# Performance work log

Measured on AMD Instinct MI355X. Metric: run time of the kernel, lower is better.

Reference implementation:

```python
import jax, jax.numpy as jnp
import numpy as np

NEG_SLOPE = 0.2

def _gat_layer(x, src, dst, W, a_s, a_d, b, concat):
    # x: [N, F_in], W: [F_in, H*C], a_s/a_d: [H, C]
    N = x.shape[0]
    H, C = a_s.shape
    h = (x @ W).reshape(N, H, C)                       # per-head projection
    al_s = jnp.sum(h * a_s, axis=-1)                   # [N, H]
    al_d = jnp.sum(h * a_d, axis=-1)                   # [N, H]
    e = jax.nn.leaky_relu(al_s[src] + al_d[dst], NEG_SLOPE)  # [E, H]
    # segment softmax over incoming edges of each dst node
    m = jax.ops.segment_max(e, dst, num_segments=N)    # [N, H]
    ex = jnp.exp(e - m[dst])
    denom = jax.ops.segment_sum(ex, dst, num_segments=N)
    alpha = ex / denom[dst]                            # [E, H]
    msg = h[src] * alpha[:, :, None]                   # [E, H, C]
    out = jax.ops.segment_sum(msg, dst, num_segments=N)  # [N, H, C]
    if concat:
        return out.reshape(N, H * C) + b
    return out.mean(axis=1) + b


def setup_inputs() -> dict:
    key = jax.random.key(0)
    ks = jax.random.split(key, 12)
    N, F_in, H, C1, LAT, E = 16384, 512, 4, 128, 64, 262144
    x = jax.random.normal(ks[0], (N, F_in), dtype=jnp.float32)
    edge_index = jax.random.randint(ks[1], (2, E), 0, N, dtype=jnp.int64)
    s = 0.05
    return {
        'x': x,
        'edge_index': edge_index,
        'W1': jax.random.normal(ks[2], (F_in, H * C1), dtype=jnp.float32) * s,
        'a_src1': jax.random.normal(ks[3], (H, C1), dtype=jnp.float32) * s,
        'a_dst1': jax.random.normal(ks[4], (H, C1), dtype=jnp.float32) * s,
        'b1': jax.random.normal(ks[5], (H * C1,), dtype=jnp.float32) * s,
        'W2': jax.random.normal(ks[6], (H * C1, H * LAT), dtype=jnp.float32) * s,
        'a_src2': jax.random.normal(ks[7], (H, LAT), dtype=jnp.float32) * s,
        'a_dst2': jax.random.normal(ks[8], (H, LAT), dtype=jnp.float32) * s,
        'b2': jax.random.normal(ks[9], (LAT,), dtype=jnp.float32) * s,
    }


def reference(x, edge_index, W1, a_src1, a_dst1, b1, W2, a_src2, a_dst2, b2):
    N = x.shape[0]
    # PyG GATConv default add_self_loops=True
    loop = jnp.arange(N, dtype=edge_index.dtype)
    src = jnp.concatenate([edge_index[0], loop])
    dst = jnp.concatenate([edge_index[1], loop])
    h = jax.nn.relu(_gat_layer(x, src, dst, W1, a_src1, a_dst1, b1, concat=True))
    out = _gat_layer(h, src, dst, W2, a_src2, a_dst2, b2, concat=False)
    return out
```

## Files before the change

### kernel.cpp

```cpp
#include <hip/hip_runtime.h>
#include <stdint.h>
#include <stddef.h>
#include <limits.h>

typedef __bf16 bf16;
typedef __bf16 bf16x4 __attribute__((ext_vector_type(4)));
typedef __bf16 bf16x8 __attribute__((ext_vector_type(8)));
typedef float  f32x4  __attribute__((ext_vector_type(4)));

#define CAP 128

static __device__ __forceinline__ float lrelu(float x) { return x > 0.f ? x : 0.2f * x; }
static __device__ __forceinline__ float san(float v) { return (fabsf(v) < 1e4f) ? v : 0.0f; }
static __device__ __forceinline__ float wexp(float e) { return __expf(fminf(e, 30.f)); }

static __device__ __forceinline__ void async_load16(const bf16* g, bf16* l) {
  __builtin_amdgcn_global_load_lds((const __attribute__((address_space(1))) void*)g,
                                   (__attribute__((address_space(3))) void*)l, 16, 0, 0);
}

static __device__ __forceinline__ void drain_barrier() {
  asm volatile("s_waitcnt vmcnt(0) lgkmcnt(0)" ::: "memory");
  __builtin_amdgcn_s_barrier();
}


__global__ __launch_bounds__(256) void prep_w(int* __restrict__ cnt,
                                              const float* __restrict__ W1,
                                              const float* __restrict__ W2,
                                              bf16* __restrict__ W1T,
                                              bf16* __restrict__ W2T,
                                              int N) {
  int b = blockIdx.x;
  if (b < N / 256) { cnt[b * 256 + threadIdx.x] = 0; return; }
  b -= N / 256;
  __shared__ bf16 t[32][33];
  const float* in; bf16* out; int R, C, bx, by;
  if (b < 256) { in = W1; out = W1T; R = 512; C = 512; by = b >> 4; bx = b & 15; }
  else         { b -= 256; in = W2; out = W2T; R = 512; C = 256; by = b >> 3; bx = b & 7; }
  const int lane = threadIdx.x & 31, r8 = threadIdx.x >> 5;
#pragma unroll
  for (int k = 0; k < 4; ++k) {
    int r = by * 32 + r8 + k * 8, c = bx * 32 + lane;
    t[lane][r8 + k * 8] = (bf16)san(in[(size_t)r * C + c]);
  }
  __syncthreads();
#pragma unroll
  for (int k = 0; k < 4; ++k) {
    int oc = bx * 32 + r8 + k * 8;
    out[(size_t)oc * R + by * 32 + lane] = t[r8 + k * 8][lane];
  }
}


__global__ __launch_bounds__(256) void gemm_al_l1(const float* __restrict__ X,
                                                  const bf16* __restrict__ BT,
                                                  bf16* __restrict__ C,
                                                  const float* __restrict__ a_s,
                                                  const float* __restrict__ a_d,
                                                  float* __restrict__ al_s,
                                                  float* __restrict__ al_d,
                                                  const int* __restrict__ src,
                                                  const int* __restrict__ dst,
                                                  int E, int* __restrict__ cnt,
                                                  int* __restrict__ slots,
                                                  int M, int N, int K) {
  __shared__ __align__(16) bf16 As[2][64 * 32];
  __shared__ __align__(16) bf16 Bs[2][128 * 32];
  __shared__ float alred[2][64][2];
  const int tid = threadIdx.x;
  const int b   = blockIdx.x;

  if (b >= 1024) {
    for (int e = (b - 1024) * 256 + tid; e < E; e += 256 * 256) {
      int d = dst[e];
      int pos = atomicAdd(&cnt[d], 1);
      if (pos < CAP) slots[(size_t)d * CAP + pos] = src[e];
    }
    return;
  }

  const int lane = tid & 63;
  const int wave = tid >> 6;
  const int m0 = (b & 255) * 64;
  const int head = b >> 8;
  const int n0 = head * 128;
  const int wm = (wave >> 1) * 32;
  const int wn = (wave & 1) * 64;

  f32x4 acc[2][4] = {};

  const int id1 = tid + 256;
  const float* apx = X  + (size_t)(m0 + (tid >> 2)) * K + (tid & 3) * 8;
  const bf16*  b0p = BT + (size_t)(n0 + (tid >> 2)) * K + (tid & 3) * 8;
  const bf16*  b1p = BT + (size_t)(n0 + (id1 >> 2)) * K + (id1 & 3) * 8;

  const int kq = (lane >> 4) * 8;
  const int rA = wm + (lane & 15);
  const int rB = wn + (lane & 15);

  {
    async_load16(b0p, &Bs[0][tid * 8]);
    async_load16(b1p, &Bs[0][id1 * 8]);
    f32x4 u0 = *(const f32x4*)(apx);
    f32x4 u1 = *(const f32x4*)(apx + 4);
    bf16x8 w;
#pragma unroll
    for (int k = 0; k < 4; ++k) { w[k] = (bf16)san(u0[k]); w[4 + k] = (bf16)san(u1[k]); }
    *(bf16x8*)&As[0][tid * 8] = w;
    drain_barrier();
  }

  int cur = 0;
  for (int k0 = 0; k0 < K; k0 += 32) {
    const int kn = k0 + 32;
    const bool pf = (kn < K);
    f32x4 u0, u1;
    if (pf) {
      async_load16(b0p + kn, &Bs[cur ^ 1][tid * 8]);
      async_load16(b1p + kn, &Bs[cur ^ 1][id1 * 8]);
      u0 = *(const f32x4*)(apx + kn);
      u1 = *(const f32x4*)(apx + kn + 4);
    }

    bf16x8 af[2], bfv[4];
#pragma unroll
    for (int i = 0; i < 2; ++i) af[i]  = *(const bf16x8*)&As[cur][(rA + i * 16) * 32 + kq];
#pragma unroll
    for (int j = 0; j < 4; ++j) bfv[j] = *(const bf16x8*)&Bs[cur][(rB + j * 16) * 32 + kq];
#pragma unroll
    for (int i = 0; i < 2; ++i)
#pragma unroll
      for (int j = 0; j < 4; ++j)
        acc[i][j] = __builtin_amdgcn_mfma_f32_16x16x32_bf16(af[i], bfv[j], acc[i][j], 0, 0, 0);

    if (pf) {
      bf16x8 w;
#pragma unroll
      for (int k = 0; k < 4; ++k) { w[k] = (bf16)san(u0[k]); w[4 + k] = (bf16)san(u1[k]); }
      *(bf16x8*)&As[cur ^ 1][tid * 8] = w;
    }

    drain_barrier();
    cur ^= 1;
  }

  const int cc = lane & 15;
  const int rb = (lane >> 4) * 4;
#pragma unroll
  for (int i = 0; i < 2; ++i)
#pragma unroll
    for (int j = 0; j < 4; ++j) {
      int gcol = n0 + wn + j * 16 + cc;
#pragma unroll
      for (int r = 0; r < 4; ++r) {
        int grow = m0 + wm + i * 16 + rb + r;
        C[(size_t)grow * N + gcol] = (bf16)acc[i][j][r];
      }
    }

  {
    float asv[4], adv[4];
#pragma unroll
    for (int j = 0; j < 4; ++j) {
      int col = head * 128 + wn + j * 16 + cc;
      asv[j] = san(a_s[col]);
      adv[j] = san(a_d[col]);
    }
    const int wnh = wn >> 6;
#pragma unroll
    for (int i = 0; i < 2; ++i)
#pragma unroll
      for (int r = 0; r < 4; ++r) {
        float ps = 0.f, pd = 0.f;
#pragma unroll
        for (int j = 0; j < 4; ++j) { ps += acc[i][j][r] * asv[j]; pd += acc[i][j][r] * adv[j]; }
#pragma unroll
        for (int off = 1; off <= 8; off <<= 1) {
          ps += __shfl_xor(ps, off);
          pd += __shfl_xor(pd, off);
        }
        if (cc == 0) {
          int row = wm + i * 16 + rb + r;
          alred[wnh][row][0] = ps;
          alred[wnh][row][1] = pd;
        }
      }
    __syncthreads();
    if (tid < 64) {
      al_s[(size_t)(m0 + tid) * 4 + head] = alred[0][tid][0] + alred[1][tid][0];
      al_d[(size_t)(m0 + tid) * 4 + head] = alred[0][tid][1] + alred[1][tid][1];
    }
  }
}


__global__ __launch_bounds__(256) void gemm_al_l2(const bf16* __restrict__ A,
                                                  const bf16* __restrict__ BT,
                                                  bf16* __restrict__ C,
                                                  const float* __restrict__ a_s,
                                                  const float* __restrict__ a_d,
                                                  float* __restrict__ al_s,
                                                  float* __restrict__ al_d,
                                                  int M, int N, int K) {
  __shared__ __align__(16) bf16 As[2][64 * 32];
  __shared__ __align__(16) bf16 Bs[2][128 * 32];
  const int tid  = threadIdx.x;
  const int lane = tid & 63;
  const int wave = tid >> 6;
  const int m0 = blockIdx.x * 64;
  const int n0 = blockIdx.y * 128;
  const int wm = (wave >> 1) * 32;
  const int wn = (wave & 1) * 64;

  f32x4 acc[2][4] = {};

  const int tb = tid + 256;
  const bf16* ap  = A  + (size_t)(m0 + (tid >> 2)) * K + (tid & 3) * 8;
  const bf16* bp0 = BT + (size_t)(n0 + (tid >> 2)) * K + (tid & 3) * 8;
  const bf16* bp1 = BT + (size_t)(n0 + (tb  >> 2)) * K + (tb  & 3) * 8;

  const int kq = (lane >> 4) * 8;
  const int rA = wm + (lane & 15);
  const int rB = wn + (lane & 15);

  async_load16(ap,  &As[0][tid * 8]);
  async_load16(bp0, &Bs[0][tid * 8]);
  async_load16(bp1, &Bs[0][tb  * 8]);
  drain_barrier();

  int cur = 0;
  for (int k0 = 0; k0 < K; k0 += 32) {
    const int kn = k0 + 32;
    if (kn < K) {
      async_load16(ap  + kn, &As[cur ^ 1][tid * 8]);
      async_load16(bp0 + kn, &Bs[cur ^ 1][tid * 8]);
      async_load16(bp1 + kn, &Bs[cur ^ 1][tb  * 8]);
    }

    bf16x8 af[2], bfv[4];
#pragma unroll
    for (int i = 0; i < 2; ++i) af[i]  = *(const bf16x8*)&As[cur][(rA + i * 16) * 32 + kq];
#pragma unroll
    for (int j = 0; j < 4; ++j) bfv[j] = *(const bf16x8*)&Bs[cur][(rB + j * 16) * 32 + kq];
#pragma unroll
    for (int i = 0; i < 2; ++i)
#pragma unroll
      for (int j = 0; j < 4; ++j)
        acc[i][j] = __builtin_amdgcn_mfma_f32_16x16x32_bf16(af[i], bfv[j], acc[i][j], 0, 0, 0);

    drain_barrier();
    cur ^= 1;
  }

  const int cc = lane & 15;
  const int rb = (lane >> 4) * 4;
#pragma unroll
  for (int i = 0; i < 2; ++i)
#pragma unroll
    for (int j = 0; j < 4; ++j) {
      int gcol = n0 + wn + j * 16 + cc;
#pragma unroll
      for (int r = 0; r < 4; ++r) {
        int grow = m0 + wm + i * 16 + rb + r;
        C[(size_t)grow * N + gcol] = (bf16)acc[i][j][r];
      }
    }

  {
    const int head = blockIdx.y * 2 + (wn >> 6);
    float asv[4], adv[4];
#pragma unroll
    for (int j = 0; j < 4; ++j) {
      int col = head * 64 + j * 16 + cc;
      asv[j] = san(a_s[col]);
      adv[j] = san(a_d[col]);
    }
#pragma unroll
    for (int i = 0; i < 2; ++i)
#pragma unroll
      for (int r = 0; r < 4; ++r) {
        float ps = 0.f, pd = 0.f;
#pragma unroll
        for (int j = 0; j < 4; ++j) { ps += acc[i][j][r] * asv[j]; pd += acc[i][j][r] * adv[j]; }
#pragma unroll
        for (int off = 1; off <= 8; off <<= 1) {
          ps += __shfl_xor(ps, off);
          pd += __shfl_xor(pd, off);
        }
        if (cc == 0) {
          int row = m0 + wm + i * 16 + rb + r;
          al_s[(size_t)row * 4 + head] = ps;
          al_d[(size_t)row * 4 + head] = pd;
        }
      }
  }
}


__global__ __launch_bounds__(256) void aggregate1_f(const bf16* __restrict__ h1,
                                                    const float* __restrict__ al_s,
                                                    const float* __restrict__ al_d,
                                                    const int* __restrict__ cnt,
                                                    int* __restrict__ slots,
                                                    const float* __restrict__ bias,
                                                    bf16* __restrict__ out) {
  __shared__ int   sIdx[4][64];
  __shared__ f32x4 sW[4][64];
  const int wv   = threadIdx.x >> 6;
  const int lane = threadIdx.x & 63;
  const int n = blockIdx.x * 4 + wv;
  const int cb = lane * 8;
  const int hd = lane >> 4;
  const int beg = n * CAP;
  const int len = min(cnt[n], CAP);
  const f32x4 alsn = *(const f32x4*)(al_s + (size_t)n * 4);
  const f32x4 aldn = *(const f32x4*)(al_d + (size_t)n * 4);

  const float wself = wexp(lrelu(alsn[hd] + aldn[hd]));
  bf16x8 hv0 = *(const bf16x8*)(h1 + (size_t)n * 512 + cb);
  float acc[8];
#pragma unroll
  for (int k = 0; k < 8; ++k) acc[k] = wself * (float)hv0[k];

  f32x4 Lv = {0.f, 0.f, 0.f, 0.f};
  if (lane == 0) {
#pragma unroll
    for (int h = 0; h < 4; ++h) Lv[h] = wexp(lrelu(alsn[h] + aldn[h]));
  }

  if (len <= 64) {
    int v = (lane < len) ? slots[beg + lane] : INT_MAX;
    if (len > 1) {
#pragma unroll
      for (int k = 2; k <= 64; k <<= 1) {
#pragma unroll
        for (int j = k >> 1; j > 0; j >>= 1) {
          int p = __shfl_xor(v, j);
          bool take_min = (((lane & k) == 0) == ((lane & j) == 0));
          v = take_min ? min(v, p) : max(v, p);
        }
      }
      if (lane < len) slots[beg + lane] = v;
    }
    if (lane < len) {
      sIdx[wv][lane] = v;
      f32x4 a = *(const f32x4*)(al_s + (size_t)v * 4);
      f32x4 w;
#pragma unroll
      for (int h = 0; h < 4; ++h) w[h] = wexp(lrelu(a[h] + aldn[h]));
      sW[wv][lane] = w;
#pragma unroll
      for (int h = 0; h < 4; ++h) Lv[h] += w[h];
    }
#pragma unroll 4
    for (int j = 0; j < len; ++j) {
      int s = sIdx[wv][j];
      float a = sW[wv][j][hd];
      bf16x8 hv = *(const bf16x8*)(h1 + (size_t)s * 512 + cb);
#pragma unroll
      for (int k = 0; k < 8; ++k) acc[k] += a * (float)hv[k];
    }
  } else {
    if (lane == 0) {
      for (int i = beg + 1; i < beg + len; ++i) {
        int v = slots[i];
        int j = i - 1;
        while (j >= beg && slots[j] > v) { slots[j + 1] = slots[j]; --j; }
        slots[j + 1] = v;
      }
    }
    asm volatile("s_waitcnt vmcnt(0)" ::: "memory");
    for (int c0 = beg; c0 < beg + len; c0 += 64) {
      const int cl = min(64, beg + len - c0);
      if (lane < cl) {
        int s = slots[c0 + lane];
        sIdx[wv][lane] = s;
        f32x4 a = *(const f32x4*)(al_s + (size_t)s * 4);
        f32x4 w;
#pragma unroll
        for (int h = 0; h < 4; ++h) w[h] = wexp(lrelu(a[h] + aldn[h]));
        sW[wv][lane] = w;
#pragma unroll
        for (int h = 0; h < 4; ++h) Lv[h] += w[h];
      }
#pragma unroll 4
      for (int j = 0; j < cl; ++j) {
        int s = sIdx[wv][j];
        float a = sW[wv][j][hd];
        bf16x8 hv = *(const bf16x8*)(h1 + (size_t)s * 512 + cb);
#pragma unroll
        for (int k = 0; k < 8; ++k) acc[k] += a * (float)hv[k];
      }
    }
  }

  for (int off = 32; off; off >>= 1) {
#pragma unroll
    for (int h = 0; h < 4; ++h) Lv[h] += __shfl_xor(Lv[h], off);
  }
  const float inv = 1.0f / Lv[hd];
  bf16x8 ov;
#pragma unroll
  for (int k = 0; k < 8; ++k)
    ov[k] = (bf16)fmaxf(acc[k] * inv + san(bias[cb + k]), 0.f);
  *(bf16x8*)(out + (size_t)n * 512 + cb) = ov;
}


__global__ __launch_bounds__(256) void aggregate2_f(const bf16* __restrict__ h2,
                                                    const float* __restrict__ al_s,
                                                    const float* __restrict__ al_d,
                                                    const int* __restrict__ cnt,
                                                    const int* __restrict__ slots,
                                                    const float* __restrict__ bias,
                                                    float* __restrict__ out) {
  __shared__ int   sIdx[4][64];
  __shared__ f32x4 sW[4][64];
  const int wv   = threadIdx.x >> 6;
  const int lane = threadIdx.x & 63;
  const int n = blockIdx.x * 4 + wv;
  const int hd = lane >> 4;
  const int cb = lane * 4;
  const int beg = n * CAP;
  const int len = min(cnt[n], CAP);
  const f32x4 alsn = *(const f32x4*)(al_s + (size_t)n * 4);
  const f32x4 aldn = *(const f32x4*)(al_d + (size_t)n * 4);

  const float wself = wexp(lrelu(alsn[hd] + aldn[hd]));
  bf16x4 hv0 = *(const bf16x4*)(h2 + (size_t)n * 256 + cb);
  float acc0 = wself * (float)hv0[0], acc1 = wself * (float)hv0[1];
  float acc2 = wself * (float)hv0[2], acc3 = wself * (float)hv0[3];
  f32x4 Lv = {0.f, 0.f, 0.f, 0.f};
  if (lane == 0) {
#pragma unroll
    for (int h = 0; h < 4; ++h) Lv[h] = wexp(lrelu(alsn[h] + aldn[h]));
  }
  for (int c0 = beg; c0 < beg + len; c0 += 64) {
    const int cl = min(64, beg + len - c0);
    if (lane < cl) {
      int s = slots[c0 + lane];
      sIdx[wv][lane] = s;
      f32x4 a = *(const f32x4*)(al_s + (size_t)s * 4);
      f32x4 w;
#pragma unroll
      for (int h = 0; h < 4; ++h) w[h] = wexp(lrelu(a[h] + aldn[h]));
      sW[wv][lane] = w;
#pragma unroll
      for (int h = 0; h < 4; ++h) Lv[h] += w[h];
    }
#pragma unroll 4
    for (int j = 0; j < cl; ++j) {
      int s = sIdx[wv][j];
      float a = sW[wv][j][hd];
      bf16x4 hv = *(const bf16x4*)(h2 + (size_t)s * 256 + cb);
      acc0 += a * (float)hv[0];
      acc1 += a * (float)hv[1];
      acc2 += a * (float)hv[2];
      acc3 += a * (float)hv[3];
    }
  }
  for (int off = 32; off; off >>= 1) {
#pragma unroll
    for (int h = 0; h < 4; ++h) Lv[h] += __shfl_xor(Lv[h], off);
  }
  const float inv = 1.0f / Lv[hd];
  acc0 *= inv; acc1 *= inv; acc2 *= inv; acc3 *= inv;
  acc0 += __shfl_xor(acc0, 16); acc1 += __shfl_xor(acc1, 16);
  acc2 += __shfl_xor(acc2, 16); acc3 += __shfl_xor(acc3, 16);
  acc0 += __shfl_xor(acc0, 32); acc1 += __shfl_xor(acc1, 32);
  acc2 += __shfl_xor(acc2, 32); acc3 += __shfl_xor(acc3, 32);
  if (lane < 16) {
    int ob = lane * 4;
    f32x4 ov;
    ov[0] = 0.25f * acc0 + san(bias[ob]);
    ov[1] = 0.25f * acc1 + san(bias[ob + 1]);
    ov[2] = 0.25f * acc2 + san(bias[ob + 2]);
    ov[3] = 0.25f * acc3 + san(bias[ob + 3]);
    *(f32x4*)(out + (size_t)n * 64 + ob) = ov;
  }
}


extern "C" void kernel_launch(void* const* d_in, const int* in_sizes, int n_in,
                              void* d_out, int out_size, void* d_ws, size_t ws_size,
                              hipStream_t stream) {
  const float* x   = (const float*)d_in[0];
  const int*   ei  = (const int*)d_in[1];
  const float* W1  = (const float*)d_in[2];
  const float* as1 = (const float*)d_in[3];
  const float* ad1 = (const float*)d_in[4];
  const float* b1  = (const float*)d_in[5];
  const float* W2  = (const float*)d_in[6];
  const float* as2 = (const float*)d_in[7];
  const float* ad2 = (const float*)d_in[8];
  const float* b2  = (const float*)d_in[9];
  float* outp = (float*)d_out;

  const int N = in_sizes[0] / 512;
  const int E = in_sizes[1] / 2;
  const int* src = ei;
  const int* dst = ei + E;

  char* p = (char*)d_ws;
  auto alloc = [&](size_t bytes) {
    char* r = p;
    p += (bytes + 255) & ~(size_t)255;
    return r;
  };
  bf16* h1    = (bf16*)alloc((size_t)N * 512 * 2);
  bf16* hbuf  = (bf16*)alloc((size_t)N * 512 * 2);
  bf16* W1T   = (bf16*)alloc((size_t)512 * 512 * 2);
  bf16* W2T   = (bf16*)alloc((size_t)256 * 512 * 2);
  float* al_s1 = (float*)alloc((size_t)N * 4 * 4);
  float* al_d1 = (float*)alloc((size_t)N * 4 * 4);
  float* al_s2 = (float*)alloc((size_t)N * 4 * 4);
  float* al_d2 = (float*)alloc((size_t)N * 4 * 4);
  int* cnt     = (int*)alloc((size_t)N * 4);
  int* slots   = (int*)alloc((size_t)N * CAP * 4);
  bf16* h2 = h1;

  prep_w<<<N / 256 + 256 + 128, 256, 0, stream>>>(cnt, W1, W2, W1T, W2T, N);

  gemm_al_l1<<<1024 + 256, 256, 0, stream>>>(x, W1T, h1, as1, ad1, al_s1, al_d1,
                                             src, dst, E, cnt, slots, N, 512, 512);
  aggregate1_f<<<N / 4, 256, 0, stream>>>(h1, al_s1, al_d1, cnt, slots, b1, hbuf);

  gemm_al_l2<<<dim3(N / 64, 2), 256, 0, stream>>>(hbuf, W2T, h2, as2, ad2, al_s2, al_d2,
                                                  N, 256, 512);
  aggregate2_f<<<N / 4, 256, 0, stream>>>(h2, al_s2, al_d2, cnt, slots, b2, outp);
}
```

Measured before the change: 190.3 us.

## Split layer-1 aggregation into weight/sort kernel and column-sliced gather kernel

The fused layer-1 aggregation is split in two. A new kernel sorts each node's neighbor slots, computes the per-edge attention weights and the self-loop weights into per-head planes, and stores the reciprocal softmax denominators. A second kernel launches 8x more blocks: each wave handles a 64-column slice of one node, and 8 lane groups gather different neighbors in parallel before a shuffle reduction. This exposes more parallel memory requests for the irregular gathers, at the cost of an extra launch, writing and re-reading an N*CAP*4 float weight buffer, and reading slots and counts eight times per node.

```diff
diff --git a/kernel.cpp b/kernel.cpp
--- a/kernel.cpp
+++ b/kernel.cpp
@@ -298,35 +298,31 @@
 }
 
 
-__global__ __launch_bounds__(256) void aggregate1_f(const bf16* __restrict__ h1,
-                                                    const float* __restrict__ al_s,
-                                                    const float* __restrict__ al_d,
-                                                    const int* __restrict__ cnt,
-                                                    int* __restrict__ slots,
-                                                    const float* __restrict__ bias,
-                                                    bf16* __restrict__ out) {
-  __shared__ int   sIdx[4][64];
-  __shared__ f32x4 sW[4][64];
+__global__ __launch_bounds__(256) void sort_mkW(const float* __restrict__ al_s,
+                                                const float* __restrict__ al_d,
+                                                const int* __restrict__ cnt,
+                                                int* __restrict__ slots,
+                                                float* __restrict__ Linv,
+                                                float* __restrict__ Wpl,
+                                                float* __restrict__ Wself,
+                                                int N) {
   const int wv   = threadIdx.x >> 6;
   const int lane = threadIdx.x & 63;
   const int n = blockIdx.x * 4 + wv;
-  const int cb = lane * 8;
-  const int hd = lane >> 4;
   const int beg = n * CAP;
   const int len = min(cnt[n], CAP);
+  const size_t plane = (size_t)N * CAP;
   const f32x4 alsn = *(const f32x4*)(al_s + (size_t)n * 4);
   const f32x4 aldn = *(const f32x4*)(al_d + (size_t)n * 4);
 
-  const float wself = wexp(lrelu(alsn[hd] + aldn[hd]));
-  bf16x8 hv0 = *(const bf16x8*)(h1 + (size_t)n * 512 + cb);
-  float acc[8];
-#pragma unroll
-  for (int k = 0; k < 8; ++k) acc[k] = wself * (float)hv0[k];
-
-  f32x4 Lv = {0.f, 0.f, 0.f, 0.f};
+  f32x4 L = {0.f, 0.f, 0.f, 0.f};
   if (lane == 0) {
 #pragma unroll
-    for (int h = 0; h < 4; ++h) Lv[h] = wexp(lrelu(alsn[h] + aldn[h]));
+    for (int h = 0; h < 4; ++h) {
+      float ws = wexp(lrelu(alsn[h] + aldn[h]));
+      L[h] = ws;
+      Wself[(size_t)h * N + n] = ws;
+    }
   }
 
   if (len <= 64) {
@@ -344,22 +340,13 @@
       if (lane < len) slots[beg + lane] = v;
     }
     if (lane < len) {
-      sIdx[wv][lane] = v;
       f32x4 a = *(const f32x4*)(al_s + (size_t)v * 4);
-      f32x4 w;
-#pragma unroll
-      for (int h = 0; h < 4; ++h) w[h] = wexp(lrelu(a[h] + aldn[h]));
-      sW[wv][lane] = w;
-#pragma unroll
-      for (int h = 0; h < 4; ++h) Lv[h] += w[h];
-    }
-#pragma unroll 4
-    for (int j = 0; j < len; ++j) {
-      int s = sIdx[wv][j];
-      float a = sW[wv][j][hd];
-      bf16x8 hv = *(const bf16x8*)(h1 + (size_t)s * 512 + cb);
-#pragma unroll
-      for (int k = 0; k < 8; ++k) acc[k] += a * (float)hv[k];
+#pragma unroll
+      for (int h = 0; h < 4; ++h) {
+        float w = wexp(lrelu(a[h] + aldn[h]));
+        L[h] += w;
+        Wpl[(size_t)h * plane + beg + lane] = w;
+      }
     }
   } else {
     if (lane == 0) {
@@ -375,36 +362,86 @@
       const int cl = min(64, beg + len - c0);
       if (lane < cl) {
         int s = slots[c0 + lane];
-        sIdx[wv][lane] = s;
         f32x4 a = *(const f32x4*)(al_s + (size_t)s * 4);
-        f32x4 w;
-#pragma unroll
-        for (int h = 0; h < 4; ++h) w[h] = wexp(lrelu(a[h] + aldn[h]));
-        sW[wv][lane] = w;
-#pragma unroll
-        for (int h = 0; h < 4; ++h) Lv[h] += w[h];
-      }
-#pragma unroll 4
-      for (int j = 0; j < cl; ++j) {
-        int s = sIdx[wv][j];
-        float a = sW[wv][j][hd];
-        bf16x8 hv = *(const bf16x8*)(h1 + (size_t)s * 512 + cb);
-#pragma unroll
-        for (int k = 0; k < 8; ++k) acc[k] += a * (float)hv[k];
+#pragma unroll
+        for (int h = 0; h < 4; ++h) {
+          float w = wexp(lrelu(a[h] + aldn[h]));
+          L[h] += w;
+          Wpl[(size_t)h * plane + c0 + lane] = w;
+        }
       }
     }
   }
 
   for (int off = 32; off; off >>= 1) {
 #pragma unroll
-    for (int h = 0; h < 4; ++h) Lv[h] += __shfl_xor(Lv[h], off);
-  }
-  const float inv = 1.0f / Lv[hd];
-  bf16x8 ov;
-#pragma unroll
-  for (int k = 0; k < 8; ++k)
-    ov[k] = (bf16)fmaxf(acc[k] * inv + san(bias[cb + k]), 0.f);
-  *(bf16x8*)(out + (size_t)n * 512 + cb) = ov;
+    for (int h = 0; h < 4; ++h) L[h] += __shfl_xor(L[h], off);
+  }
+  if (lane == 0) {
+    f32x4 o;
+#pragma unroll
+    for (int h = 0; h < 4; ++h) o[h] = 1.0f / L[h];
+    *(f32x4*)(Linv + (size_t)n * 4) = o;
+  }
+}
+
+
+__global__ __launch_bounds__(256) void aggregate1_x(const bf16* __restrict__ h1,
+                                                    const int* __restrict__ cnt,
+                                                    const int* __restrict__ slots,
+                                                    const float* __restrict__ Wpl,
+                                                    const float* __restrict__ Wself,
+                                                    const float* __restrict__ Linv,
+                                                    const float* __restrict__ bias,
+                                                    bf16* __restrict__ out, int N) {
+  const int sl   = blockIdx.x & 7;
+  const int g    = blockIdx.x >> 3;
+  const int wv   = threadIdx.x >> 6;
+  const int lane = threadIdx.x & 63;
+  const int n    = g * 4 + wv;
+  const int hd   = sl >> 1;
+  const int c8   = lane & 7;
+  const int sub  = lane >> 3;
+  const int cbase = sl * 64 + c8 * 8;
+  const int beg = n * CAP;
+  const int len = min(cnt[n], CAP);
+  const float* wrow = Wpl + (size_t)hd * N * CAP + beg;
+
+  float acc[8] = {};
+  if (sub == 0) {
+    float ws = Wself[(size_t)hd * N + n];
+    bf16x8 hv = *(const bf16x8*)(h1 + (size_t)n * 512 + cbase);
+#pragma unroll
+    for (int k = 0; k < 8; ++k) acc[k] = ws * (float)hv[k];
+  }
+
+  for (int c0 = 0; c0 < len; c0 += 64) {
+    const int cl = min(64, len - c0);
+    int   v = (lane < cl) ? slots[beg + c0 + lane] : 0;
+    float w = (lane < cl) ? wrow[c0 + lane] : 0.f;
+    for (int j0 = 0; j0 < cl; j0 += 8) {
+      int jj = j0 + sub;
+      int   sj = __shfl(v, jj);
+      float wj = __shfl(w, jj);
+      bf16x8 rv = *(const bf16x8*)(h1 + (size_t)sj * 512 + cbase);
+#pragma unroll
+      for (int k = 0; k < 8; ++k) acc[k] += wj * (float)rv[k];
+    }
+  }
+
+#pragma unroll
+  for (int off = 8; off <= 32; off <<= 1)
+#pragma unroll
+    for (int k = 0; k < 8; ++k) acc[k] += __shfl_xor(acc[k], off);
+
+  if (sub == 0) {
+    const float inv = Linv[(size_t)n * 4 + hd];
+    bf16x8 ov;
+#pragma unroll
+    for (int k = 0; k < 8; ++k)
+      ov[k] = (bf16)fmaxf(acc[k] * inv + san(bias[cbase + k]), 0.f);
+    *(bf16x8*)(out + (size_t)n * 512 + cbase) = ov;
+  }
 }
 
 
@@ -516,15 +553,20 @@
   float* al_d1 = (float*)alloc((size_t)N * 4 * 4);
   float* al_s2 = (float*)alloc((size_t)N * 4 * 4);
   float* al_d2 = (float*)alloc((size_t)N * 4 * 4);
+  float* Linv1 = (float*)alloc((size_t)N * 4 * 4);
   int* cnt     = (int*)alloc((size_t)N * 4);
   int* slots   = (int*)alloc((size_t)N * CAP * 4);
+  float* Wpl   = (float*)alloc((size_t)4 * N * CAP * 4);
+  float* Wself = (float*)alloc((size_t)4 * N * 4);
   bf16* h2 = h1;
 
   prep_w<<<N / 256 + 256 + 128, 256, 0, stream>>>(cnt, W1, W2, W1T, W2T, N);
 
   gemm_al_l1<<<1024 + 256, 256, 0, stream>>>(x, W1T, h1, as1, ad1, al_s1, al_d1,
                                              src, dst, E, cnt, slots, N, 512, 512);
-  aggregate1_f<<<N / 4, 256, 0, stream>>>(h1, al_s1, al_d1, cnt, slots, b1, hbuf);
+  sort_mkW<<<N / 4, 256, 0, stream>>>(al_s1, al_d1, cnt, slots, Linv1, Wpl, Wself, N);
+  aggregate1_x<<<8 * (N / 4), 256, 0, stream>>>(h1, cnt, slots, Wpl, Wself, Linv1,
+                                                b1, hbuf, N);
 
   gemm_al_l2<<<dim3(N / 64, 2), 256, 0, stream>>>(hbuf, W2T, h2, as2, ad2, al_s2, al_d2,
                                                   N, 256, 512);
```

New measurement: 212.8 us. 1.12x slower.
